# Kernel tuning notes

Hardware: AMD Instinct MI355X
Metric: run time of the kernel (lower is better)

Reference implementation:

```python
import jax, jax.numpy as jnp
import numpy as np

N, D, E, R, TOPK = 8192, 4096, 8, 128, 2
LORA_ALPHA = 32.0
SCALING = LORA_ALPHA / R


def setup_inputs() -> dict:
    key = jax.random.key(0)
    kx, kr, ka, kb = jax.random.split(key, 4)
    x = jax.random.normal(kx, (N, D), jnp.float32)
    Wr = jax.random.normal(kr, (E, D), jnp.float32) * 0.02  # router Linear weight [E, D]
    br = jnp.zeros((E,), jnp.float32)                        # router bias
    A = jax.random.normal(ka, (E, R, D), jnp.float32) * 0.02  # per-expert lora_A weights
    B = jax.random.normal(kb, (E, D, R), jnp.float32) * 0.02  # per-expert lora_B weights
    return {"x": x, "Wr": Wr, "br": br, "A": A, "B": B}


def reference(x, Wr, br, A, B):
    # Router: softmax over expert logits, top-k, renormalize selected probs.
    logits = x @ Wr.T + br                       # [N, E]
    probs = jax.nn.softmax(logits, axis=-1)
    top_v, top_i = jax.lax.top_k(probs, TOPK)    # [N, K]
    w = top_v / jnp.sum(top_v, axis=-1, keepdims=True)
    # Scatter renormalized weights back to a dense [N, E] gate (0 for unselected).
    n_idx = jnp.arange(x.shape[0])[:, None]
    gate = jnp.zeros_like(probs).at[n_idx, top_i].set(w)
    # Expert LoRA: y_e = (x @ A_e^T) @ B_e^T * scaling; combine with gates.
    h = jnp.einsum('nd,erd->ner', x, A)          # [N, E, R] small rank intermediate
    out = jnp.einsum('ner,ne,eor->no', h, gate, B) * SCALING  # [N, D]
    return out
```

## Files before the change

kernel.cpp:

```cpp
#include <hip/hip_runtime.h>

#define N_TOK 8192
#define DIM   4096
#define NEXP  8
#define RANK  128
#define EK    (NEXP * RANK)
#define SCAL  0.25f

typedef unsigned short u16;
typedef __bf16 bf16x8 __attribute__((ext_vector_type(8)));
typedef float  f32x4  __attribute__((ext_vector_type(4)));

typedef const __attribute__((address_space(1))) void* as1_cvp;
typedef __attribute__((address_space(3))) void*       as3_vp;

__device__ __forceinline__ void async16(void* lds, const void* g) {
  __builtin_amdgcn_global_load_lds((as1_cvp)g, (as3_vp)lds, 16, 0, 0);
}

__device__ __forceinline__ u16 f2bf(float f) {
  unsigned int u = __builtin_bit_cast(unsigned int, f);
  u += 0x7fffu + ((u >> 16) & 1u);
  return (u16)(u >> 16);
}

__device__ __forceinline__ f32x4 mfma16(bf16x8 a, bf16x8 b, f32x4 c) {
  return __builtin_amdgcn_mfma_f32_16x16x32_bf16(a, b, c, 0, 0, 0);
}

#define PIPE_WAIT(N)                                            \
  __builtin_amdgcn_sched_barrier(0);                            \
  asm volatile("s_waitcnt vmcnt(" #N ")" ::: "memory");         \
  __builtin_amdgcn_s_barrier();                                 \
  __builtin_amdgcn_sched_barrier(0)

#define PIPE_END()                                              \
  __builtin_amdgcn_sched_barrier(0);                            \
  __builtin_amdgcn_s_barrier();                                 \
  __builtin_amdgcn_sched_barrier(0)

__global__ __launch_bounds__(256) void cvtA_kernel(const float* __restrict__ A,
                                                   u16* __restrict__ Ab) {
  size_t i = (size_t)blockIdx.x * 256 + threadIdx.x;
  float4 v = ((const float4*)A)[i];
  ushort4 o;
  o.x = f2bf(v.x); o.y = f2bf(v.y); o.z = f2bf(v.z); o.w = f2bf(v.w);
  ((ushort4*)Ab)[i] = o;
}

__global__ __launch_bounds__(256) void cvtB_kernel(const float* __restrict__ B,
                                                   u16* __restrict__ Bt) {
  size_t i = (size_t)blockIdx.x * 256 + threadIdx.x;
  int r4 = (int)(i & 31);
  int o_ = (int)((i >> 5) & 4095);
  int e  = (int)(i >> 17);
  float4 v = ((const float4*)B)[i];
  ushort4 u;
  u.x = f2bf(v.x); u.y = f2bf(v.y); u.z = f2bf(v.z); u.w = f2bf(v.w);
  ((ushort4*)Bt)[(size_t)o_ * 256 + e * 32 + r4] = u;
}

__device__ __forceinline__ void router_finalize(
    int n, const float* l_in, const float* __restrict__ br,
    float* __restrict__ gw, int* __restrict__ sel) {
  float l[NEXP];
#pragma unroll
  for (int e = 0; e < NEXP; ++e) l[e] = l_in[e] + br[e];
  int i0 = 0;
#pragma unroll
  for (int e = 1; e < NEXP; ++e) if (l[e] > l[i0]) i0 = e;
  int i1 = (i0 == 0) ? 1 : 0;
#pragma unroll
  for (int e = 0; e < NEXP; ++e) if (e != i0 && l[e] > l[i1]) i1 = e;
  float w0 = 1.f / (1.f + expf(l[i1] - l[i0]));
  gw[n * 2 + 0] = w0 * SCAL;
  gw[n * 2 + 1] = (1.f - w0) * SCAL;
  sel[n] = i0 | (i1 << 4);
}

#define R_STAGE(kc, buf)                                                    \
  {                                                                         \
    const int k0_ = (kc) * 512;                                             \
    _Pragma("unroll")                                                       \
    for (int r_ = 0; r_ < 4; ++r_)                                          \
      async16(&WrL[buf][r_ * 1024 + tid * 4],                               \
              wsrc + (size_t)(2 * r_) * DIM + k0_);                         \
  }

#define R_LOADX(kc, xv)                                                     \
  {                                                                         \
    const int kb_ = (kc) * 128;                                             \
    _Pragma("unroll")                                                       \
    for (int t_ = 0; t_ < 4; ++t_)                                          \
      _Pragma("unroll")                                                     \
      for (int c_ = 0; c_ < 2; ++c_)                                        \
        xv[t_][c_] = x4[(size_t)(tok0 + t_) * 1024 + kb_ + c_ * 64 + lane]; \
  }

#define R_COMPUTE(kc, buf, xv)                                              \
  {                                                                         \
    const float4* WL_ = (const float4*)WrL[buf];                            \
    _Pragma("unroll")                                                       \
    for (int c_ = 0; c_ < 2; ++c_) {                                        \
      float4 wr_[8];                                                        \
      _Pragma("unroll")                                                     \
      for (int e_ = 0; e_ < 8; ++e_)                                        \
        wr_[e_] = WL_[e_ * 128 + c_ * 64 + lane];                           \
      _Pragma("unroll")                                                     \
      for (int t_ = 0; t_ < 4; ++t_)                                        \
        _Pragma("unroll")                                                   \
        for (int e_ = 0; e_ < 8; ++e_)                                      \
          sums[t_][e_] += xv[t_][c_].x * wr_[e_].x + xv[t_][c_].y * wr_[e_].y + \
                          xv[t_][c_].z * wr_[e_].z + xv[t_][c_].w * wr_[e_].w;  \
    }                                                                       \
    const int kb_ = (kc) * 128;                                             \
    _Pragma("unroll")                                                       \
    for (int t_ = 0; t_ < 4; ++t_) {                                        \
      ushort4* xo_ = (ushort4*)(xb + (size_t)(tok0 + t_) * DIM);            \
      _Pragma("unroll")                                                     \
      for (int c_ = 0; c_ < 2; ++c_) {                                      \
        float4 v_ = xv[t_][c_];                                             \
        ushort4 o_;                                                         \
        o_.x = f2bf(v_.x); o_.y = f2bf(v_.y);                               \
        o_.z = f2bf(v_.z); o_.w = f2bf(v_.w);                               \
        xo_[kb_ + c_ * 64 + lane] = o_;                                     \
      }                                                                     \
    }                                                                       \
  }

__global__ __launch_bounds__(256, 2) void router_kernel(
    const float* __restrict__ x, const float* __restrict__ Wr,
    const float* __restrict__ br, u16* __restrict__ xb,
    float* __restrict__ gw, int* __restrict__ sel) {
  __shared__ alignas(16) float WrL[2][4096];

  const int tid = threadIdx.x;
  const int wv = tid >> 6, lane = tid & 63;
  const int tok0 = blockIdx.x * 16 + wv * 4;

  const float4* x4 = (const float4*)x;
  const float* wsrc = Wr + (size_t)(tid >> 7) * DIM + (tid & 127) * 4;

  float4 xvA[4][2], xvB[4][2];
  float sums[4][8] = {};

  R_STAGE(0, 0); R_LOADX(0, xvA);
  for (int kc = 0; kc < 3; ++kc) {
    R_STAGE(2 * kc + 1, 1); R_LOADX(2 * kc + 1, xvB);
    PIPE_WAIT(12);
    R_COMPUTE(2 * kc, 0, xvA);
    PIPE_END();
    R_STAGE(2 * kc + 2, 0); R_LOADX(2 * kc + 2, xvA);
    PIPE_WAIT(12);
    R_COMPUTE(2 * kc + 1, 1, xvB);
    PIPE_END();
  }
  R_STAGE(7, 1); R_LOADX(7, xvB);
  PIPE_WAIT(12);
  R_COMPUTE(6, 0, xvA);
  PIPE_END();
  PIPE_WAIT(0);
  R_COMPUTE(7, 1, xvB);

#pragma unroll
  for (int m = 1; m < 64; m <<= 1)
#pragma unroll
    for (int t = 0; t < 4; ++t)
#pragma unroll
      for (int e = 0; e < 8; ++e)
        sums[t][e] += __shfl_xor(sums[t][e], m, 64);

  if (lane < 4) {
    float fl[8];
#pragma unroll
    for (int e = 0; e < 8; ++e)
      fl[e] = lane == 0 ? sums[0][e]
            : lane == 1 ? sums[1][e]
            : lane == 2 ? sums[2][e] : sums[3][e];
    router_finalize(tok0 + lane, fl, br, gw, sel);
  }
}

__global__ __launch_bounds__(512) void listbuild_kernel(
    const int* __restrict__ sel, int* __restrict__ lists,
    int* __restrict__ cnt) {
  __shared__ int blkCnt[NEXP];
  __shared__ int gBase[NEXP];
  __shared__ int waveOff[8][NEXP];
  const int tid = threadIdx.x;
  const int wv = tid >> 6, lane = tid & 63;
  const int n = blockIdx.x * 512 + tid;
  if (tid < NEXP) blkCnt[tid] = 0;
  __syncthreads();
  const int s = sel[n];
  const int i0 = s & 15, i1 = (s >> 4) & 15;
#pragma unroll
  for (int e = 0; e < NEXP; ++e) {
    unsigned long long m0 = __ballot(i0 == e);
    unsigned long long m1 = __ballot(i1 == e);
    if (lane == 0)
      waveOff[wv][e] = atomicAdd(&blkCnt[e], __popcll(m0) + __popcll(m1));
  }
  __syncthreads();
  if (tid < NEXP) gBase[tid] = atomicAdd(&cnt[tid], blkCnt[tid]);
  __syncthreads();
  const unsigned long long lt = (1ull << lane) - 1;
#pragma unroll
  for (int e = 0; e < NEXP; ++e) {
    unsigned long long m0 = __ballot(i0 == e);
    unsigned long long m1 = __ballot(i1 == e);
    int base = gBase[e] + waveOff[wv][e];
    if (i0 == e) lists[e * N_TOK + base + (int)__popcll(m0 & lt)] = n * 2;
    if (i1 == e)
      lists[e * N_TOK + base + (int)__popcll(m0) + (int)__popcll(m1 & lt)] =
          n * 2 + 1;
  }
}

__global__ __launch_bounds__(256) void gemm1_kernel(
    const u16* __restrict__ xb, const u16* __restrict__ Ab,
    const int* __restrict__ lists, const int* __restrict__ cnt,
    const float* __restrict__ gw, u16* __restrict__ G) {
  const int e = blockIdx.y;
  const int mt = blockIdx.x;
  const int c = cnt[e];
  if (mt * 64 >= c) return;

  __shared__ alignas(16) u16 ringA[4][64 * 32];
  __shared__ alignas(16) u16 ringB[4][128 * 32];
  __shared__ int   tokS[64];
  __shared__ float wS[64];

  const int tid = threadIdx.x;
  if (tid < 64) {
    int idx = mt * 64 + tid;
    int ci = idx < c ? idx : (c - 1);
    int entry = lists[e * N_TOK + ci];
    tokS[tid] = entry >> 1;
    wS[tid] = (idx < c) ? gw[entry] : 0.0f;
  }
  __syncthreads();

  const int srow = tid >> 2;
  const int scol = (tid & 3) * 8;
  const u16* gA  = xb + (size_t)tokS[srow] * DIM + scol;
  const u16* gB0 = Ab + (size_t)e * (RANK * DIM) + (size_t)srow * DIM + scol;
  const u16* gB1 = gB0 + (size_t)64 * DIM;

  const int lane = tid & 63, wvi = tid >> 6;
  const int wm = wvi >> 1, wn = wvi & 1;
  const int m16 = lane & 15, quad = lane >> 4;

  f32x4 acc[2][4] = {};

  auto STAGE = [&](int kt, int slot) {
    const int k0 = kt * 32;
    async16(&ringA[slot][tid * 8],        gA  + k0);
    async16(&ringB[slot][tid * 8],        gB0 + k0);
    async16(&ringB[slot][tid * 8 + 2048], gB1 + k0);
  };

  auto COMPUTE = [&](int slot) {
    bf16x8 af[2], bfr[4];
#pragma unroll
    for (int j = 0; j < 4; ++j)
      bfr[j] = *(const bf16x8*)&ringB[slot][(wn * 64 + j * 16 + m16) * 32 + quad * 8];
#pragma unroll
    for (int i = 0; i < 2; ++i)
      af[i] = *(const bf16x8*)&ringA[slot][(wm * 32 + i * 16 + m16) * 32 + quad * 8];
    __builtin_amdgcn_s_setprio(1);
#pragma unroll
    for (int i = 0; i < 2; ++i)
#pragma unroll
      for (int j = 0; j < 4; ++j) acc[i][j] = mfma16(af[i], bfr[j], acc[i][j]);
    __builtin_amdgcn_s_setprio(0);
  };

  STAGE(0, 0);
  STAGE(1, 1);
  STAGE(2, 2);

  for (int t = 0; t < 125; ++t) {
    PIPE_WAIT(6);
    STAGE(t + 3, (t + 3) & 3);
    COMPUTE(t & 3);
    PIPE_END();
  }
  PIPE_WAIT(6); COMPUTE(1); PIPE_END();
  PIPE_WAIT(3); COMPUTE(2); PIPE_END();
  PIPE_WAIT(0); COMPUTE(3); PIPE_END();

#pragma unroll
  for (int i = 0; i < 2; ++i)
#pragma unroll
    for (int rr = 0; rr < 4; ++rr) {
      int row = wm * 32 + i * 16 + quad * 4 + rr;
      if (mt * 64 + row < c) {
        int tk = tokS[row];
        float wgt = wS[row];
        u16* gp = G + (size_t)tk * EK + e * RANK + wn * 64 + m16;
#pragma unroll
        for (int j = 0; j < 4; ++j) gp[j * 16] = f2bf(acc[i][j][rr] * wgt);
      }
    }
}

__global__ __launch_bounds__(512, 2) void gemm2_kernel(
    const u16* __restrict__ G, const u16* __restrict__ Bt,
    float* __restrict__ out) {
  __shared__ alignas(16) u16 ring[4][2][256 * 32];

  const int lin = blockIdx.y * 16 + blockIdx.x;
  const int swz = (lin & 7) * 64 + (lin >> 3);
  const int by = swz >> 4;
  const int bx = swz & 15;

  const int tid = threadIdx.x;
  const int sr = tid >> 2;
  const int sc = (tid & 3) * 8;
  const u16* gA = G  + (size_t)(by * 256 + sr) * EK + sc;
  const u16* gB = Bt + (size_t)(bx * 256 + sr) * EK + sc;

  const int lane = tid & 63, wvi = tid >> 6;
  const int wm = wvi >> 2, wn = wvi & 3;
  const int m16 = lane & 15, quad = lane >> 4;

  f32x4 acc[8][4] = {};

  auto STAGE = [&](int kt, int slot) {
    u16* lA = &ring[slot][0][tid * 8];
    u16* lB = &ring[slot][1][tid * 8];
    const u16* sA = gA + kt * 32;
    const u16* sB = gB + kt * 32;
    async16(lA,        sA);
    async16(lA + 4096, sA + (size_t)128 * EK);
    async16(lB,        sB);
    async16(lB + 4096, sB + (size_t)128 * EK);
  };

  auto COMPUTE = [&](int slot) {
    const u16* As_ = &ring[slot][0][0];
    const u16* Bs_ = &ring[slot][1][0];
    bf16x8 bfr[4];
#pragma unroll
    for (int j = 0; j < 4; ++j)
      bfr[j] = *(const bf16x8*)&Bs_[(wn * 64 + j * 16 + m16) * 32 + quad * 8];
    __builtin_amdgcn_s_setprio(1);
#pragma unroll
    for (int i = 0; i < 8; ++i) {
      bf16x8 af = *(const bf16x8*)&As_[(wm * 128 + i * 16 + m16) * 32 + quad * 8];
#pragma unroll
      for (int j = 0; j < 4; ++j) acc[i][j] = mfma16(af, bfr[j], acc[i][j]);
    }
    __builtin_amdgcn_s_setprio(0);
  };

  STAGE(0, 0);
  STAGE(1, 1);
  STAGE(2, 2);

  for (int t = 0; t < 29; ++t) {
    PIPE_WAIT(8);
    STAGE(t + 3, (t + 3) & 3);
    COMPUTE(t & 3);
    PIPE_END();
  }
  PIPE_WAIT(8); COMPUTE(1); PIPE_END();
  PIPE_WAIT(4); COMPUTE(2); PIPE_END();
  PIPE_WAIT(0); COMPUTE(3); PIPE_END();

#pragma unroll
  for (int i = 0; i < 8; ++i)
#pragma unroll
    for (int rr = 0; rr < 4; ++rr) {
      int row = by * 256 + wm * 128 + i * 16 + quad * 4 + rr;
      float* op = out + (size_t)row * DIM + bx * 256 + wn * 64 + m16;
#pragma unroll
      for (int j = 0; j < 4; ++j) op[j * 16] = acc[i][j][rr];
    }
}

extern "C" void kernel_launch(void* const* d_in, const int* in_sizes, int n_in,
                              void* d_out, int out_size, void* d_ws, size_t ws_size,
                              hipStream_t stream) {
  const float* x  = (const float*)d_in[0];
  const float* Wr = (const float*)d_in[1];
  const float* br = (const float*)d_in[2];
  const float* A  = (const float*)d_in[3];
  const float* B  = (const float*)d_in[4];
  float* out = (float*)d_out;

  char* w = (char*)d_ws;
  u16* xb = (u16*)w;      w += (size_t)N_TOK * DIM * 2;
  u16* G  = (u16*)w;      w += (size_t)N_TOK * EK * 2;
  u16* Ab = (u16*)w;      w += (size_t)NEXP * RANK * DIM * 2;
  u16* Bt = (u16*)w;      w += (size_t)DIM * EK * 2;
  float* gw = (float*)w;  w += (size_t)N_TOK * 2 * 4;
  int* lists = (int*)w;   w += (size_t)NEXP * N_TOK * 4;
  int* sel = (int*)w;     w += (size_t)N_TOK * 4;
  int* cnt = (int*)w;     w += 256;

  hipMemsetAsync(cnt, 0, NEXP * sizeof(int), stream);
  hipMemsetAsync(G, 0, (size_t)N_TOK * EK * 2, stream);

  cvtA_kernel<<<dim3(4096), dim3(256), 0, stream>>>(A, Ab);
  cvtB_kernel<<<dim3(4096), dim3(256), 0, stream>>>(B, Bt);
  router_kernel<<<dim3(512), dim3(256), 0, stream>>>(x, Wr, br, xb, gw, sel);
  listbuild_kernel<<<dim3(16), dim3(512), 0, stream>>>(sel, lists, cnt);
  gemm1_kernel<<<dim3(128, NEXP), dim3(256), 0, stream>>>(xb, Ab, lists, cnt, gw, G);
  gemm2_kernel<<<dim3(16, 32), dim3(512), 0, stream>>>(G, Bt, out);
}
```

Baseline: 446.3 us.

## Halve router tokens per wave and widen gemm1 K-tile with swizzled LDS

The router now handles 2 tokens per wave instead of 4 and launches twice as many blocks. This gives more parallelism and lower register pressure, at the cost of staging the router weights twice as often. In gemm1 the K-step per pipeline stage doubles from 32 to 64, halving the number of loop iterations and barriers. LDS tiles use an XOR swizzle on column groups to avoid bank conflicts, with the wait counts adjusted to match. The larger ring uses twice the LDS, which may reduce occupancy.

```diff
diff --git a/kernel.cpp b/kernel.cpp
--- a/kernel.cpp
+++ b/kernel.cpp
@@ -91,7 +91,7 @@
   {                                                                         \
     const int kb_ = (kc) * 128;                                             \
     _Pragma("unroll")                                                       \
-    for (int t_ = 0; t_ < 4; ++t_)                                          \
+    for (int t_ = 0; t_ < 2; ++t_)                                          \
       _Pragma("unroll")                                                     \
       for (int c_ = 0; c_ < 2; ++c_)                                        \
         xv[t_][c_] = x4[(size_t)(tok0 + t_) * 1024 + kb_ + c_ * 64 + lane]; \
@@ -107,7 +107,7 @@
       for (int e_ = 0; e_ < 8; ++e_)                                        \
         wr_[e_] = WL_[e_ * 128 + c_ * 64 + lane];                           \
       _Pragma("unroll")                                                     \
-      for (int t_ = 0; t_ < 4; ++t_)                                        \
+      for (int t_ = 0; t_ < 2; ++t_)                                        \
         _Pragma("unroll")                                                   \
         for (int e_ = 0; e_ < 8; ++e_)                                      \
           sums[t_][e_] += xv[t_][c_].x * wr_[e_].x + xv[t_][c_].y * wr_[e_].y + \
@@ -115,7 +115,7 @@
     }                                                                       \
     const int kb_ = (kc) * 128;                                             \
     _Pragma("unroll")                                                       \
-    for (int t_ = 0; t_ < 4; ++t_) {                                        \
+    for (int t_ = 0; t_ < 2; ++t_) {                                        \
       ushort4* xo_ = (ushort4*)(xb + (size_t)(tok0 + t_) * DIM);            \
       _Pragma("unroll")                                                     \
       for (int c_ = 0; c_ < 2; ++c_) {                                      \
@@ -136,27 +136,27 @@
 
   const int tid = threadIdx.x;
   const int wv = tid >> 6, lane = tid & 63;
-  const int tok0 = blockIdx.x * 16 + wv * 4;
+  const int tok0 = blockIdx.x * 8 + wv * 2;
 
   const float4* x4 = (const float4*)x;
   const float* wsrc = Wr + (size_t)(tid >> 7) * DIM + (tid & 127) * 4;
 
-  float4 xvA[4][2], xvB[4][2];
-  float sums[4][8] = {};
+  float4 xvA[2][2], xvB[2][2];
+  float sums[2][8] = {};
 
   R_STAGE(0, 0); R_LOADX(0, xvA);
   for (int kc = 0; kc < 3; ++kc) {
     R_STAGE(2 * kc + 1, 1); R_LOADX(2 * kc + 1, xvB);
-    PIPE_WAIT(12);
+    PIPE_WAIT(8);
     R_COMPUTE(2 * kc, 0, xvA);
     PIPE_END();
     R_STAGE(2 * kc + 2, 0); R_LOADX(2 * kc + 2, xvA);
-    PIPE_WAIT(12);
+    PIPE_WAIT(8);
     R_COMPUTE(2 * kc + 1, 1, xvB);
     PIPE_END();
   }
   R_STAGE(7, 1); R_LOADX(7, xvB);
-  PIPE_WAIT(12);
+  PIPE_WAIT(8);
   R_COMPUTE(6, 0, xvA);
   PIPE_END();
   PIPE_WAIT(0);
@@ -165,18 +165,16 @@
 #pragma unroll
   for (int m = 1; m < 64; m <<= 1)
 #pragma unroll
-    for (int t = 0; t < 4; ++t)
+    for (int t = 0; t < 2; ++t)
 #pragma unroll
       for (int e = 0; e < 8; ++e)
         sums[t][e] += __shfl_xor(sums[t][e], m, 64);
 
-  if (lane < 4) {
+  if (lane < 2) {
     float fl[8];
 #pragma unroll
     for (int e = 0; e < 8; ++e)
-      fl[e] = lane == 0 ? sums[0][e]
-            : lane == 1 ? sums[1][e]
-            : lane == 2 ? sums[2][e] : sums[3][e];
+      fl[e] = (lane == 0) ? sums[0][e] : sums[1][e];
     router_finalize(tok0 + lane, fl, br, gw, sel);
   }
 }
@@ -226,8 +224,8 @@
   const int c = cnt[e];
   if (mt * 64 >= c) return;
 
-  __shared__ alignas(16) u16 ringA[4][64 * 32];
-  __shared__ alignas(16) u16 ringB[4][128 * 32];
+  __shared__ alignas(16) u16 ringA[4][64 * 64];
+  __shared__ alignas(16) u16 ringB[4][128 * 64];
   __shared__ int   tokS[64];
   __shared__ float wS[64];
 
@@ -241,54 +239,62 @@
   }
   __syncthreads();
 
-  const int srow = tid >> 2;
-  const int scol = (tid & 3) * 8;
-  const u16* gA  = xb + (size_t)tokS[srow] * DIM + scol;
-  const u16* gB0 = Ab + (size_t)e * (RANK * DIM) + (size_t)srow * DIM + scol;
-  const u16* gB1 = gB0 + (size_t)64 * DIM;
+  const int srow = tid >> 3;
+  const int cg   = tid & 7;
+  const int cgs  = cg ^ (srow & 7);
+  const u16* gA0 = xb + (size_t)tokS[srow] * DIM + cgs * 8;
+  const u16* gA1 = xb + (size_t)tokS[srow + 32] * DIM + cgs * 8;
+  const u16* gB0 = Ab + (size_t)e * (RANK * DIM) + (size_t)srow * DIM + cgs * 8;
 
   const int lane = tid & 63, wvi = tid >> 6;
   const int wm = wvi >> 1, wn = wvi & 1;
   const int m16 = lane & 15, quad = lane >> 4;
+  const int swz = m16 & 7;
 
   f32x4 acc[2][4] = {};
 
   auto STAGE = [&](int kt, int slot) {
-    const int k0 = kt * 32;
-    async16(&ringA[slot][tid * 8],        gA  + k0);
-    async16(&ringB[slot][tid * 8],        gB0 + k0);
-    async16(&ringB[slot][tid * 8 + 2048], gB1 + k0);
+    const int k0 = kt * 64;
+    async16(&ringA[slot][tid * 8],        gA0 + k0);
+    async16(&ringA[slot][tid * 8 + 2048], gA1 + k0);
+#pragma unroll
+    for (int r = 0; r < 4; ++r)
+      async16(&ringB[slot][tid * 8 + r * 2048], gB0 + (size_t)r * 32 * DIM + k0);
   };
 
   auto COMPUTE = [&](int slot) {
-    bf16x8 af[2], bfr[4];
-#pragma unroll
-    for (int j = 0; j < 4; ++j)
-      bfr[j] = *(const bf16x8*)&ringB[slot][(wn * 64 + j * 16 + m16) * 32 + quad * 8];
-#pragma unroll
-    for (int i = 0; i < 2; ++i)
-      af[i] = *(const bf16x8*)&ringA[slot][(wm * 32 + i * 16 + m16) * 32 + quad * 8];
-    __builtin_amdgcn_s_setprio(1);
-#pragma unroll
-    for (int i = 0; i < 2; ++i)
-#pragma unroll
-      for (int j = 0; j < 4; ++j) acc[i][j] = mfma16(af[i], bfr[j], acc[i][j]);
-    __builtin_amdgcn_s_setprio(0);
+#pragma unroll
+    for (int ks = 0; ks < 2; ++ks) {
+      const int off = ((ks * 4 + quad) ^ swz) * 8;
+      bf16x8 af[2], bfr[4];
+#pragma unroll
+      for (int j = 0; j < 4; ++j)
+        bfr[j] = *(const bf16x8*)&ringB[slot][(wn * 64 + j * 16 + m16) * 64 + off];
+#pragma unroll
+      for (int i = 0; i < 2; ++i)
+        af[i] = *(const bf16x8*)&ringA[slot][(wm * 32 + i * 16 + m16) * 64 + off];
+      __builtin_amdgcn_s_setprio(1);
+#pragma unroll
+      for (int i = 0; i < 2; ++i)
+#pragma unroll
+        for (int j = 0; j < 4; ++j) acc[i][j] = mfma16(af[i], bfr[j], acc[i][j]);
+      __builtin_amdgcn_s_setprio(0);
+    }
   };
 
   STAGE(0, 0);
   STAGE(1, 1);
   STAGE(2, 2);
 
-  for (int t = 0; t < 125; ++t) {
-    PIPE_WAIT(6);
+  for (int t = 0; t < 61; ++t) {
+    PIPE_WAIT(12);
     STAGE(t + 3, (t + 3) & 3);
     COMPUTE(t & 3);
     PIPE_END();
   }
-  PIPE_WAIT(6); COMPUTE(1); PIPE_END();
-  PIPE_WAIT(3); COMPUTE(2); PIPE_END();
-  PIPE_WAIT(0); COMPUTE(3); PIPE_END();
+  PIPE_WAIT(12); COMPUTE(1); PIPE_END();
+  PIPE_WAIT(6);  COMPUTE(2); PIPE_END();
+  PIPE_WAIT(0);  COMPUTE(3); PIPE_END();
 
 #pragma unroll
   for (int i = 0; i < 2; ++i)
@@ -405,7 +411,7 @@
 
   cvtA_kernel<<<dim3(4096), dim3(256), 0, stream>>>(A, Ab);
   cvtB_kernel<<<dim3(4096), dim3(256), 0, stream>>>(B, Bt);
-  router_kernel<<<dim3(512), dim3(256), 0, stream>>>(x, Wr, br, xb, gw, sel);
+  router_kernel<<<dim3(1024), dim3(256), 0, stream>>>(x, Wr, br, xb, gw, sel);
   listbuild_kernel<<<dim3(16), dim3(512), 0, stream>>>(sel, lists, cnt);
   gemm1_kernel<<<dim3(128, NEXP), dim3(256), 0, stream>>>(xb, Ab, lists, cnt, gw, G);
   gemm2_kernel<<<dim3(16, 32), dim3(512), 0, stream>>>(G, Bt, out);
```

Result: no change. 441.4 us (-1.1%).
